# Optimization experiments

Measured on AMD Instinct MI355X. Metric: run time of the kernel, lower is better.

Reference implementation:

```python
import jax, jax.numpy as jnp
import numpy as np
import math

H = 128
W = 128
N = 2048
DIM = 768
TWO_PI = 2.0 * math.pi
ALPHA_MIN = 1.0 / 255.0


def setup_inputs() -> dict:
    key = jax.random.key(0)
    ks = jax.random.split(key, 6)
    # _xyz = atanh(2*(rand-0.5)); clip uniform away from endpoints to avoid inf
    u = jax.random.uniform(ks[0], (N, 2), minval=1e-4, maxval=1.0 - 1e-4)
    xyz = jnp.arctanh(2.0 * (u - 0.5))
    scaling = jax.random.uniform(ks[1], (N, 2))
    rotation = jax.random.uniform(ks[2], (N, 1))
    features = jax.random.uniform(ks[3], (N, 3))
    opacity = jnp.ones((N, 1), jnp.float32)
    w_up = jax.random.normal(ks[4], (DIM, 3), jnp.float32) * 0.05
    b_up = jnp.zeros((DIM,), jnp.float32)
    x = jax.random.normal(ks[5], (1, DIM, H, W), jnp.float32)
    return {"x": x, "xyz": xyz, "scaling": scaling, "rotation": rotation,
            "features": features, "opacity": opacity, "w_up": w_up, "b_up": b_up}


def _forward(xyz, scaling, rotation, features, opacity, w_up, b_up):
    # activations (get_xyz / get_scaling / get_rotation)
    means = jnp.tanh(xyz)                                   # [N,2] in (-1,1)
    s = jnp.abs(scaling + 0.5)                              # [N,2]
    theta = jax.nn.sigmoid(rotation[:, 0]) * TWO_PI         # [N]
    c, sn = jnp.cos(theta), jnp.sin(theta)
    # M = R(theta) @ diag(s); cov2d = M M^T
    a = c * s[:, 0]; b = -sn * s[:, 1]
    d = sn * s[:, 0]; e = c * s[:, 1]
    cov_xx = a * a + b * b
    cov_xy = a * d + b * e
    cov_yy = d * d + e * e
    det = cov_xx * cov_yy - cov_xy * cov_xy
    # conic = inverse covariance (A, B, C)
    A = cov_yy / det; B = -cov_xy / det; C = cov_xx / det   # [N]
    # project [-1,1] -> pixel centers
    gx = 0.5 * (means[:, 0] + 1.0) * W                      # [N]
    gy = 0.5 * (means[:, 1] + 1.0) * H
    px = jnp.arange(W, dtype=jnp.float32) + 0.5
    py = jnp.arange(H, dtype=jnp.float32) + 0.5
    PX, PY = jnp.meshgrid(px, py)                           # [H,W], PX varies along W
    dx = gx[None, :] - PX.reshape(-1)[:, None]              # [P,N], P=H*W
    dy = gy[None, :] - PY.reshape(-1)[:, None]
    sigma = 0.5 * (A * dx * dx + C * dy * dy) + B * dx * dy # [P,N]
    alpha = jnp.minimum(0.999, opacity[:, 0][None, :] * jnp.exp(-sigma))
    alpha = jnp.where((sigma < 0.0) | (alpha < ALPHA_MIN), 0.0, alpha)
    # summation rasterizer: per-pixel weighted sum of colors
    img = jnp.clip(alpha @ features, 0.0, 1.0)              # [P,3]
    feat = img @ w_up.T + b_up                              # [P,DIM]
    return feat.T.reshape(1, DIM, H, W)


def reference(x, xyz, scaling, rotation, features, opacity, w_up, b_up):
    del x  # only its channel dim (== DIM) shapes the output in the original
    return _forward(xyz, scaling, rotation, features, opacity, w_up, b_up)
```

## Files before the change

### kernel.cpp

```cpp
#include <hip/hip_runtime.h>
#include <math.h>

#define HH 128
#define WW 128
#define NG 2048
#define DIMV 768
#define PIX (HH * WW)
#define A_MIN (1.0f / 255.0f)
#define TW 16
#define TH 4

__global__ __launch_bounds__(256) void prep_kernel(
    const float* __restrict__ xyz, const float* __restrict__ scaling,
    const float* __restrict__ rotation, const float* __restrict__ features,
    const float* __restrict__ opacity,
    float4* __restrict__ q0, float4* __restrict__ q1, float2* __restrict__ q2)
{
    int n = blockIdx.x * 256 + threadIdx.x;
    if (n >= NG) return;
    float mx = tanhf(xyz[2 * n + 0]);
    float my = tanhf(xyz[2 * n + 1]);
    float gx = 0.5f * (mx + 1.0f) * (float)WW;
    float gy = 0.5f * (my + 1.0f) * (float)HH;
    float s0 = fabsf(scaling[2 * n + 0] + 0.5f);
    float s1 = fabsf(scaling[2 * n + 1] + 0.5f);
    float th = 6.28318530717958647692f / (1.0f + expf(-rotation[n]));
    float sn, cs;
    sincosf(th, &sn, &cs);
    float a = cs * s0, b = -sn * s1, d = sn * s0, e = cs * s1;
    float cxx = a * a + b * b;
    float cxy = a * d + b * e;
    float cyy = d * d + e * e;
    float det = cxx * cyy - cxy * cxy;
    float inv = 1.0f / det;
    float A = cyy * inv, B = -cxy * inv, C = cxx * inv;
    float op = opacity[n];
    float L = logf(255.0f * op);
    float r2 = (L > 0.0f) ? (2.0f * L * (cxx + cyy)) * 1.0002f + 1e-3f : -1.0f;
    q0[n] = make_float4(0.5f * A, B, 0.5f * C, op);
    q1[n] = make_float4(gx, gy, features[3 * n + 0], features[3 * n + 1]);
    q2[n] = make_float2(features[3 * n + 2], r2);
}

__global__ __launch_bounds__(256) void raster_kernel(
    const float4* __restrict__ q0, const float4* __restrict__ q1,
    const float2* __restrict__ q2, const float* __restrict__ w_up,
    const float* __restrict__ b_up, float* __restrict__ out)
{
    __shared__ int s_cnt;
    __shared__ int s_list[NG];
    __shared__ float s_red[4 * 64 * 3];
    __shared__ float s_img[64 * 3];
    __shared__ float4 s_wub[DIMV];

    int tid = threadIdx.x;
    int bx = blockIdx.x & 7, by = blockIdx.x >> 3;
    int px0 = bx * TW, py0 = by * TH;

    if (tid == 0) s_cnt = 0;
    __syncthreads();

    {
        float x0 = px0 + 0.5f, x1 = px0 + TW - 0.5f;
        float y0 = py0 + 0.5f, y1 = py0 + TH - 0.5f;
        for (int g = tid; g < NG; g += 256) {
            float4 c1 = q1[g];
            float2 c2 = q2[g];
            float ddx = fmaxf(fmaxf(x0 - c1.x, c1.x - x1), 0.0f);
            float ddy = fmaxf(fmaxf(y0 - c1.y, c1.y - y1), 0.0f);
            if (ddx * ddx + ddy * ddy <= c2.y) {
                int pos = atomicAdd(&s_cnt, 1);
                s_list[pos] = g;
            }
        }
    }
    for (int dd = tid; dd < DIMV; dd += 256) {
        s_wub[dd] = make_float4(w_up[3 * dd + 0], w_up[3 * dd + 1],
                                w_up[3 * dd + 2], b_up[dd]);
    }
    __syncthreads();
    int cnt = s_cnt;

    int lane = tid & 63, wv = tid >> 6;
    float pxf = px0 + (lane & 15) + 0.5f;
    float pyf = py0 + (lane >> 4) + 0.5f;

    float ar = 0.0f, ag = 0.0f, ab = 0.0f;
    for (int k = wv; k < cnt; k += 4) {
        int g = __builtin_amdgcn_readfirstlane(s_list[k]);
        float4 a0 = q0[g];
        float4 a1 = q1[g];
        float2 a2 = q2[g];
        float dx = a1.x - pxf, dy = a1.y - pyf;
        float sig = fmaf(a0.y * dx, dy, fmaf(a0.x * dx, dx, a0.z * dy * dy));
        float al = fminf(0.999f, a0.w * __expf(-sig));
        al = (sig < 0.0f || al < A_MIN) ? 0.0f : al;
        ar = fmaf(al, a1.z, ar);
        ag = fmaf(al, a1.w, ag);
        ab = fmaf(al, a2.x, ab);
    }
    s_red[(wv * 64 + lane) * 3 + 0] = ar;
    s_red[(wv * 64 + lane) * 3 + 1] = ag;
    s_red[(wv * 64 + lane) * 3 + 2] = ab;
    __syncthreads();

    if (tid < 64) {
        float sr = 0.0f, sg = 0.0f, sb = 0.0f;
        for (int w = 0; w < 4; ++w) {
            sr += s_red[(w * 64 + tid) * 3 + 0];
            sg += s_red[(w * 64 + tid) * 3 + 1];
            sb += s_red[(w * 64 + tid) * 3 + 2];
        }
        s_img[tid * 3 + 0] = fminf(1.0f, fmaxf(0.0f, sr));
        s_img[tid * 3 + 1] = fminf(1.0f, fmaxf(0.0f, sg));
        s_img[tid * 3 + 2] = fminf(1.0f, fmaxf(0.0f, sb));
    }
    __syncthreads();

    int sub = lane >> 4;
    int r4 = (lane >> 2) & 3;
    int cq = lane & 3;
    int pi = r4 * TW + cq * 4;
    float i00 = s_img[(pi + 0) * 3 + 0], i01 = s_img[(pi + 0) * 3 + 1], i02 = s_img[(pi + 0) * 3 + 2];
    float i10 = s_img[(pi + 1) * 3 + 0], i11 = s_img[(pi + 1) * 3 + 1], i12 = s_img[(pi + 1) * 3 + 2];
    float i20 = s_img[(pi + 2) * 3 + 0], i21 = s_img[(pi + 2) * 3 + 1], i22 = s_img[(pi + 2) * 3 + 2];
    float i30 = s_img[(pi + 3) * 3 + 0], i31 = s_img[(pi + 3) * 3 + 1], i32 = s_img[(pi + 3) * 3 + 2];
    size_t base = (size_t)(py0 + r4) * WW + (size_t)(px0 + cq * 4);
    #pragma unroll 4
    for (int rnd = 0; rnd < DIMV / 16; ++rnd) {
        int dd = rnd * 16 + wv * 4 + sub;
        float4 wb = s_wub[dd];
        float4 v;
        v.x = fmaf(wb.x, i00, fmaf(wb.y, i01, fmaf(wb.z, i02, wb.w)));
        v.y = fmaf(wb.x, i10, fmaf(wb.y, i11, fmaf(wb.z, i12, wb.w)));
        v.z = fmaf(wb.x, i20, fmaf(wb.y, i21, fmaf(wb.z, i22, wb.w)));
        v.w = fmaf(wb.x, i30, fmaf(wb.y, i31, fmaf(wb.z, i32, wb.w)));
        *(float4*)(out + (size_t)dd * PIX + base) = v;
    }
}

extern "C" void kernel_launch(void* const* d_in, const int* in_sizes, int n_in,
                              void* d_out, int out_size, void* d_ws, size_t ws_size,
                              hipStream_t stream)
{
    const float* xyz      = (const float*)d_in[1];
    const float* scaling  = (const float*)d_in[2];
    const float* rotation = (const float*)d_in[3];
    const float* features = (const float*)d_in[4];
    const float* opacity  = (const float*)d_in[5];
    const float* w_up     = (const float*)d_in[6];
    const float* b_up     = (const float*)d_in[7];
    float* out = (float*)d_out;

    float4* q0 = (float4*)d_ws;
    float4* q1 = q0 + NG;
    float2* q2 = (float2*)(q1 + NG);

    prep_kernel<<<NG / 256, 256, 0, stream>>>(xyz, scaling, rotation, features,
                                              opacity, q0, q1, q2);
    raster_kernel<<<256, 256, 0, stream>>>(q0, q1, q2, w_up, b_up, out);
}
```

Before: 129.6 us.

## Fuse gaussian prep into raster blocks and split projection into wide grid

```diff
diff --git a/kernel.cpp b/kernel.cpp
--- a/kernel.cpp
+++ b/kernel.cpp
@@ -9,63 +9,57 @@
 #define A_MIN (1.0f / 255.0f)
 #define TW 16
 #define TH 4
+#define TWO_PI 6.28318530717958647692f
 
-__global__ __launch_bounds__(256) void prep_kernel(
+__global__ __launch_bounds__(256) void raster_kernel(
     const float* __restrict__ xyz, const float* __restrict__ scaling,
     const float* __restrict__ rotation, const float* __restrict__ features,
-    const float* __restrict__ opacity,
-    float4* __restrict__ q0, float4* __restrict__ q1, float2* __restrict__ q2)
+    const float* __restrict__ opacity, float* __restrict__ img)
 {
-    int n = blockIdx.x * 256 + threadIdx.x;
-    if (n >= NG) return;
-    float mx = tanhf(xyz[2 * n + 0]);
-    float my = tanhf(xyz[2 * n + 1]);
-    float gx = 0.5f * (mx + 1.0f) * (float)WW;
-    float gy = 0.5f * (my + 1.0f) * (float)HH;
-    float s0 = fabsf(scaling[2 * n + 0] + 0.5f);
-    float s1 = fabsf(scaling[2 * n + 1] + 0.5f);
-    float th = 6.28318530717958647692f / (1.0f + expf(-rotation[n]));
-    float sn, cs;
-    sincosf(th, &sn, &cs);
-    float a = cs * s0, b = -sn * s1, d = sn * s0, e = cs * s1;
-    float cxx = a * a + b * b;
-    float cxy = a * d + b * e;
-    float cyy = d * d + e * e;
-    float det = cxx * cyy - cxy * cxy;
-    float inv = 1.0f / det;
-    float A = cyy * inv, B = -cxy * inv, C = cxx * inv;
-    float op = opacity[n];
-    float L = logf(255.0f * op);
-    float r2 = (L > 0.0f) ? (2.0f * L * (cxx + cyy)) * 1.0002f + 1e-3f : -1.0f;
-    q0[n] = make_float4(0.5f * A, B, 0.5f * C, op);
-    q1[n] = make_float4(gx, gy, features[3 * n + 0], features[3 * n + 1]);
-    q2[n] = make_float2(features[3 * n + 2], r2);
-}
-
-__global__ __launch_bounds__(256) void raster_kernel(
-    const float4* __restrict__ q0, const float4* __restrict__ q1,
-    const float2* __restrict__ q2, const float* __restrict__ w_up,
-    const float* __restrict__ b_up, float* __restrict__ out)
-{
+    __shared__ float4 sP0[NG];
+    __shared__ float4 sP1[NG];
+    __shared__ float2 sP2[NG];
     __shared__ int s_cnt;
     __shared__ int s_list[NG];
     __shared__ float s_red[4 * 64 * 3];
-    __shared__ float s_img[64 * 3];
-    __shared__ float4 s_wub[DIMV];
 
     int tid = threadIdx.x;
     int bx = blockIdx.x & 7, by = blockIdx.x >> 3;
     int px0 = bx * TW, py0 = by * TH;
 
     if (tid == 0) s_cnt = 0;
+
+    for (int g = tid; g < NG; g += 256) {
+        float2 xz = ((const float2*)xyz)[g];
+        float e2x = __expf(2.0f * xz.x);
+        float e2y = 2.0f * __expf(2.0f * xz.y);
+        float gx = (e2x / (e2x + 1.0f)) * (float)WW;
+        float gy = (e2y / (e2y + 2.0f)) * (float)HH;
+        float2 sc = ((const float2*)scaling)[g];
+        float s0 = fabsf(sc.x + 0.5f);
+        float s1 = fabsf(sc.y + 0.5f);
+        float th = TWO_PI / (1.0f + __expf(-rotation[g]));
+        float sn = __sinf(th), cs = __cosf(th);
+        float a = cs * s0, b = -sn * s1, d = sn * s0, e = cs * s1;
+        float cxx = a * a + b * b;
+        float cxy = a * d + b * e;
+        float cyy = d * d + e * e;
+        float inv = 1.0f / (cxx * cyy - cxy * cxy);
+        float op = opacity[g];
+        float L = __logf(255.0f * op);
+        float r2 = (L > 0.0f) ? 2.0f * L * (cxx + cyy) * 1.0002f + 1e-3f : -1.0f;
+        sP0[g] = make_float4(0.5f * cyy * inv, -cxy * inv, 0.5f * cxx * inv, op);
+        sP1[g] = make_float4(gx, gy, features[3 * g + 0], features[3 * g + 1]);
+        sP2[g] = make_float2(features[3 * g + 2], r2);
+    }
     __syncthreads();
 
     {
         float x0 = px0 + 0.5f, x1 = px0 + TW - 0.5f;
         float y0 = py0 + 0.5f, y1 = py0 + TH - 0.5f;
         for (int g = tid; g < NG; g += 256) {
-            float4 c1 = q1[g];
-            float2 c2 = q2[g];
+            float4 c1 = sP1[g];
+            float2 c2 = sP2[g];
             float ddx = fmaxf(fmaxf(x0 - c1.x, c1.x - x1), 0.0f);
             float ddy = fmaxf(fmaxf(y0 - c1.y, c1.y - y1), 0.0f);
             if (ddx * ddx + ddy * ddy <= c2.y) {
@@ -73,10 +67,6 @@
                 s_list[pos] = g;
             }
         }
-    }
-    for (int dd = tid; dd < DIMV; dd += 256) {
-        s_wub[dd] = make_float4(w_up[3 * dd + 0], w_up[3 * dd + 1],
-                                w_up[3 * dd + 2], b_up[dd]);
     }
     __syncthreads();
     int cnt = s_cnt;
@@ -88,9 +78,9 @@
     float ar = 0.0f, ag = 0.0f, ab = 0.0f;
     for (int k = wv; k < cnt; k += 4) {
         int g = __builtin_amdgcn_readfirstlane(s_list[k]);
-        float4 a0 = q0[g];
-        float4 a1 = q1[g];
-        float2 a2 = q2[g];
+        float4 a0 = sP0[g];
+        float4 a1 = sP1[g];
+        float2 a2 = sP2[g];
         float dx = a1.x - pxf, dy = a1.y - pyf;
         float sig = fmaf(a0.y * dx, dy, fmaf(a0.x * dx, dx, a0.z * dy * dy));
         float al = fminf(0.999f, a0.w * __expf(-sig));
@@ -106,36 +96,41 @@
 
     if (tid < 64) {
         float sr = 0.0f, sg = 0.0f, sb = 0.0f;
+        #pragma unroll
         for (int w = 0; w < 4; ++w) {
             sr += s_red[(w * 64 + tid) * 3 + 0];
             sg += s_red[(w * 64 + tid) * 3 + 1];
             sb += s_red[(w * 64 + tid) * 3 + 2];
         }
-        s_img[tid * 3 + 0] = fminf(1.0f, fmaxf(0.0f, sr));
-        s_img[tid * 3 + 1] = fminf(1.0f, fmaxf(0.0f, sg));
-        s_img[tid * 3 + 2] = fminf(1.0f, fmaxf(0.0f, sb));
+        int p = (py0 + (tid >> 4)) * WW + px0 + (tid & 15);
+        img[p]           = fminf(1.0f, fmaxf(0.0f, sr));
+        img[PIX + p]     = fminf(1.0f, fmaxf(0.0f, sg));
+        img[2 * PIX + p] = fminf(1.0f, fmaxf(0.0f, sb));
     }
-    __syncthreads();
+}
 
-    int sub = lane >> 4;
-    int r4 = (lane >> 2) & 3;
-    int cq = lane & 3;
-    int pi = r4 * TW + cq * 4;
-    float i00 = s_img[(pi + 0) * 3 + 0], i01 = s_img[(pi + 0) * 3 + 1], i02 = s_img[(pi + 0) * 3 + 2];
-    float i10 = s_img[(pi + 1) * 3 + 0], i11 = s_img[(pi + 1) * 3 + 1], i12 = s_img[(pi + 1) * 3 + 2];
-    float i20 = s_img[(pi + 2) * 3 + 0], i21 = s_img[(pi + 2) * 3 + 1], i22 = s_img[(pi + 2) * 3 + 2];
-    float i30 = s_img[(pi + 3) * 3 + 0], i31 = s_img[(pi + 3) * 3 + 1], i32 = s_img[(pi + 3) * 3 + 2];
-    size_t base = (size_t)(py0 + r4) * WW + (size_t)(px0 + cq * 4);
-    #pragma unroll 4
-    for (int rnd = 0; rnd < DIMV / 16; ++rnd) {
-        int dd = rnd * 16 + wv * 4 + sub;
-        float4 wb = s_wub[dd];
+__global__ __launch_bounds__(256) void project_kernel(
+    const float* __restrict__ img, const float* __restrict__ w_up,
+    const float* __restrict__ b_up, float* __restrict__ out)
+{
+    int grp = blockIdx.x >> 4;
+    int seg = blockIdx.x & 15;
+    int p = seg * 1024 + threadIdx.x * 4;
+    float4 r = *(const float4*)(img + p);
+    float4 g = *(const float4*)(img + PIX + p);
+    float4 b = *(const float4*)(img + 2 * PIX + p);
+    int d0 = grp * 4;
+    #pragma unroll
+    for (int i = 0; i < 4; ++i) {
+        int d = d0 + i;
+        float w0 = w_up[3 * d + 0], w1 = w_up[3 * d + 1], w2 = w_up[3 * d + 2];
+        float bb = b_up[d];
         float4 v;
-        v.x = fmaf(wb.x, i00, fmaf(wb.y, i01, fmaf(wb.z, i02, wb.w)));
-        v.y = fmaf(wb.x, i10, fmaf(wb.y, i11, fmaf(wb.z, i12, wb.w)));
-        v.z = fmaf(wb.x, i20, fmaf(wb.y, i21, fmaf(wb.z, i22, wb.w)));
-        v.w = fmaf(wb.x, i30, fmaf(wb.y, i31, fmaf(wb.z, i32, wb.w)));
-        *(float4*)(out + (size_t)dd * PIX + base) = v;
+        v.x = fmaf(w0, r.x, fmaf(w1, g.x, fmaf(w2, b.x, bb)));
+        v.y = fmaf(w0, r.y, fmaf(w1, g.y, fmaf(w2, b.y, bb)));
+        v.z = fmaf(w0, r.z, fmaf(w1, g.z, fmaf(w2, b.z, bb)));
+        v.w = fmaf(w0, r.w, fmaf(w1, g.w, fmaf(w2, b.w, bb)));
+        *(float4*)(out + (size_t)d * PIX + p) = v;
     }
 }
 
@@ -151,12 +146,9 @@
     const float* w_up     = (const float*)d_in[6];
     const float* b_up     = (const float*)d_in[7];
     float* out = (float*)d_out;
+    float* img = (float*)d_ws;
 
-    float4* q0 = (float4*)d_ws;
-    float4* q1 = q0 + NG;
-    float2* q2 = (float2*)(q1 + NG);
-
-    prep_kernel<<<NG / 256, 256, 0, stream>>>(xyz, scaling, rotation, features,
-                                              opacity, q0, q1, q2);
-    raster_kernel<<<256, 256, 0, stream>>>(q0, q1, q2, w_up, b_up, out);
+    raster_kernel<<<256, 256, 0, stream>>>(xyz, scaling, rotation, features,
+                                           opacity, img);
+    project_kernel<<<(DIMV / 4) * 16, 256, 0, stream>>>(img, w_up, b_up, out);
 }
```

After: 114.3 us. 1.13x faster.
